# Optimization experiments

Hardware: AMD Instinct MI355X
Metric: run time of the kernel (lower is better)

## Reference

```python
import jax, jax.numpy as jnp
import numpy as np

PNUM = 1024

def _smooth_l1(d):
    ad = jnp.abs(d)
    return jnp.where(ad < 1.0, 0.5 * d * d, ad - 0.5)

def setup_inputs() -> dict:
    key = jax.random.key(0)
    k1, k2 = jax.random.split(key)
    B = 128
    pred = jax.random.normal(k1, (B, PNUM, 2), dtype=jnp.float32)
    gt = jax.random.normal(k2, (B, PNUM, 2), dtype=jnp.float32)
    return {"pred": pred, "gt": gt}

def reference(pred, gt):
    pnum = pred.shape[1]
    # idx[i, j] = (j + i) % pnum : all cyclic shifts of gt point ordering
    idx = (jnp.arange(pnum)[:, None] + jnp.arange(pnum)[None, :]) % pnum
    gt_expand = gt[:, idx, :]                 # [B, pnum, pnum, 2]
    diff = pred[:, None, :, :] - gt_expand    # broadcast over shift axis
    dis = _smooth_l1(diff).sum(axis=3).mean(axis=2)  # [B, pnum]
    min_dis = jnp.min(dis, axis=1)            # [B]; per-sample mean of [1,1] is itself
    return jnp.mean(min_dis)
```

## Files before the change

### kernel.cpp

```cpp
#include <hip/hip_runtime.h>

#define PNUM 1024
#define NB   128
#define PAD(k) ((k) + ((k) >> 2))

typedef _Float16 h2 __attribute__((ext_vector_type(2)));

#define SL1(acc, p, g) do {                               \
    h2 d_ = (p) - (g);                                    \
    h2 a_ = __builtin_elementwise_abs(d_);                \
    h2 m_ = __builtin_elementwise_min(a_, one2);          \
    h2 t_ = __builtin_elementwise_fma(m_, nh2, a_);       \
    (acc) = __builtin_elementwise_fma(m_, t_, (acc)); } while (0)

static __device__ __forceinline__ h2 to_h2(float2 f) {
  h2 r; r.x = (_Float16)f.x; r.y = (_Float16)f.y; return r;
}

__global__ __launch_bounds__(256) void poly_cost_kernel(
    const float* __restrict__ pred, const float* __restrict__ gt,
    float* __restrict__ block_min) {
  __shared__ h2    pred_s[1280];
  __shared__ h2    gt_s[1360];
  __shared__ float partial[16][64];

  const int b     = blockIdx.x >> 4;
  const int chunk = blockIdx.x & 15;
  const int t     = threadIdx.x;

  const float2* pred2 = (const float2*)(pred + (size_t)b * (PNUM * 2));
  const float2* gt2   = (const float2*)(gt   + (size_t)b * (PNUM * 2));

  #pragma unroll
  for (int k = t; k < PNUM; k += 256)
    pred_s[PAD(k)] = to_h2(pred2[k]);
  const int gb = chunk * 64;
  for (int k = t; k < 1088; k += 256)
    gt_s[PAD(k)] = to_h2(gt2[(gb + k) & (PNUM - 1)]);
  __syncthreads();

  const int sslot = t & 15;
  const int jslot = t >> 4;
  const int kbase = sslot * 4 + jslot * 64;
  int A = PAD(kbase);
  int P = PAD(jslot * 64);

  const h2 one2 = { (_Float16)1.0f,  (_Float16)1.0f };
  const h2 nh2  = { (_Float16)-0.5f, (_Float16)-0.5f };
  h2 acc0 = { (_Float16)0.0f, (_Float16)0.0f };
  h2 acc1 = acc0, acc2 = acc0, acc3 = acc0;

  h2 w0 = gt_s[A], w1 = gt_s[A + 1], w2 = gt_s[A + 2];

  for (int g = 0; g < 16; ++g) {
    h2 p0 = pred_s[P];
    h2 w3 = gt_s[A + 3];
    SL1(acc0, p0, w0); SL1(acc1, p0, w1); SL1(acc2, p0, w2); SL1(acc3, p0, w3);
    h2 p1 = pred_s[P + 1];
    h2 n0 = gt_s[A + 5];
    SL1(acc0, p1, w1); SL1(acc1, p1, w2); SL1(acc2, p1, w3); SL1(acc3, p1, n0);
    h2 p2 = pred_s[P + 2];
    h2 n1 = gt_s[A + 6];
    SL1(acc0, p2, w2); SL1(acc1, p2, w3); SL1(acc2, p2, n0); SL1(acc3, p2, n1);
    h2 p3 = pred_s[P + 3];
    h2 n2 = gt_s[A + 7];
    SL1(acc0, p3, w3); SL1(acc1, p3, n0); SL1(acc2, p3, n1); SL1(acc3, p3, n2);
    w0 = n0; w1 = n1; w2 = n2;
    A += 5; P += 5;
  }

  {
    const int ls = sslot * 4;
    partial[jslot][ls + 0] = (float)acc0.x + (float)acc0.y;
    partial[jslot][ls + 1] = (float)acc1.x + (float)acc1.y;
    partial[jslot][ls + 2] = (float)acc2.x + (float)acc2.y;
    partial[jslot][ls + 3] = (float)acc3.x + (float)acc3.y;
  }
  __syncthreads();

  if (t < 64) {
    float s = 0.0f;
    #pragma unroll
    for (int q = 0; q < 16; ++q) s += partial[q][t];
    float dis = s * (1.0f / 1024.0f);
    #pragma unroll
    for (int off = 32; off; off >>= 1)
      dis = fminf(dis, __shfl_xor(dis, off));
    if (t == 0) block_min[blockIdx.x] = dis;
  }
}

__global__ __launch_bounds__(128) void poly_reduce_kernel(
    const float* __restrict__ block_min, float* __restrict__ out) {
  const int b = threadIdx.x;
  float m = block_min[b * 16];
  #pragma unroll
  for (int c = 1; c < 16; ++c) m = fminf(m, block_min[b * 16 + c]);
  #pragma unroll
  for (int off = 32; off; off >>= 1) m += __shfl_xor(m, off);
  __shared__ float wsum[2];
  if ((b & 63) == 0) wsum[b >> 6] = m;
  __syncthreads();
  if (b == 0) out[0] = (wsum[0] + wsum[1]) * (1.0f / NB);
}

extern "C" void kernel_launch(void* const* d_in, const int* in_sizes, int n_in,
                              void* d_out, int out_size, void* d_ws, size_t ws_size,
                              hipStream_t stream) {
  const float* pred = (const float*)d_in[0];
  const float* gt   = (const float*)d_in[1];
  float* out        = (float*)d_out;
  float* block_min  = (float*)d_ws;

  poly_cost_kernel<<<NB * 16, 256, 0, stream>>>(pred, gt, block_min);
  poly_reduce_kernel<<<1, 128, 0, stream>>>(block_min, out);
}
```

Baseline: 29.32 us.

## Fuse final reduction into cost kernel via last-block atomic counter

Replaces the separate reduction kernel launch with a last-block-done pattern: each block publishes its minimum with a release store and increments an atomic counter, and the final block performs the batch mean. The pred shared-memory layout also changes to 66-stride rows so each thread reads its four pred values with two 8-byte vector loads instead of four scalar loads. This removes a kernel launch and trims LDS instructions, but adds a memset before the kernel, an atomic per block and an extra barrier.

```diff
diff --git a/kernel.cpp b/kernel.cpp
--- a/kernel.cpp
+++ b/kernel.cpp
@@ -1,10 +1,13 @@
 #include <hip/hip_runtime.h>
 
-#define PNUM 1024
-#define NB   128
-#define PAD(k) ((k) + ((k) >> 2))
+#define PNUM    1024
+#define NB      128
+#define NBLOCKS (NB * 16)
 
 typedef _Float16 h2 __attribute__((ext_vector_type(2)));
+typedef _Float16 h4 __attribute__((ext_vector_type(4)));
+
+#define PAD(k) ((k) + ((k) >> 2))
 
 #define SL1(acc, p, g) do {                               \
     h2 d_ = (p) - (g);                                    \
@@ -17,12 +20,14 @@
   h2 r; r.x = (_Float16)f.x; r.y = (_Float16)f.y; return r;
 }
 
-__global__ __launch_bounds__(256) void poly_cost_kernel(
+__global__ __launch_bounds__(256) void poly_kernel(
     const float* __restrict__ pred, const float* __restrict__ gt,
-    float* __restrict__ block_min) {
-  __shared__ h2    pred_s[1280];
+    float* __restrict__ block_min, unsigned* __restrict__ counter,
+    float* __restrict__ out) {
+  __shared__ h2    pred_s[1054];
   __shared__ h2    gt_s[1360];
   __shared__ float partial[16][64];
+  __shared__ int   lastflag;
 
   const int b     = blockIdx.x >> 4;
   const int chunk = blockIdx.x & 15;
@@ -33,7 +38,7 @@
 
   #pragma unroll
   for (int k = t; k < PNUM; k += 256)
-    pred_s[PAD(k)] = to_h2(pred2[k]);
+    pred_s[66 * (k >> 6) + (k & 63)] = to_h2(pred2[k]);
   const int gb = chunk * 64;
   for (int k = t; k < 1088; k += 256)
     gt_s[PAD(k)] = to_h2(gt2[(gb + k) & (PNUM - 1)]);
@@ -41,40 +46,38 @@
 
   const int sslot = t & 15;
   const int jslot = t >> 4;
-  const int kbase = sslot * 4 + jslot * 64;
-  int A = PAD(kbase);
-  int P = PAD(jslot * 64);
+  const h2* Pp = pred_s + 66 * jslot;
+  const h2* Gp = gt_s + PAD(4 * sslot + 64 * jslot);
 
-  const h2 one2 = { (_Float16)1.0f,  (_Float16)1.0f };
-  const h2 nh2  = { (_Float16)-0.5f, (_Float16)-0.5f };
-  h2 acc0 = { (_Float16)0.0f, (_Float16)0.0f };
-  h2 acc1 = acc0, acc2 = acc0, acc3 = acc0;
+  const h2 one2 = {(_Float16)1.0f,  (_Float16)1.0f};
+  const h2 nh2  = {(_Float16)-0.5f, (_Float16)-0.5f};
+  h2 a0 = {(_Float16)0.0f, (_Float16)0.0f};
+  h2 a1 = a0, a2 = a0, a3 = a0;
 
-  h2 w0 = gt_s[A], w1 = gt_s[A + 1], w2 = gt_s[A + 2];
+  h2 w0 = Gp[0], w1 = Gp[1], w2 = Gp[2];
 
   for (int g = 0; g < 16; ++g) {
-    h2 p0 = pred_s[P];
-    h2 w3 = gt_s[A + 3];
-    SL1(acc0, p0, w0); SL1(acc1, p0, w1); SL1(acc2, p0, w2); SL1(acc3, p0, w3);
-    h2 p1 = pred_s[P + 1];
-    h2 n0 = gt_s[A + 5];
-    SL1(acc0, p1, w1); SL1(acc1, p1, w2); SL1(acc2, p1, w3); SL1(acc3, p1, n0);
-    h2 p2 = pred_s[P + 2];
-    h2 n1 = gt_s[A + 6];
-    SL1(acc0, p2, w2); SL1(acc1, p2, w3); SL1(acc2, p2, n0); SL1(acc3, p2, n1);
-    h2 p3 = pred_s[P + 3];
-    h2 n2 = gt_s[A + 7];
-    SL1(acc0, p3, w3); SL1(acc1, p3, n0); SL1(acc2, p3, n1); SL1(acc3, p3, n2);
+    h4 pa = *(const h4*)(Pp);
+    h4 pb = *(const h4*)(Pp + 2);
+    h2 p0 = pa.xy, p1 = pa.zw, p2 = pb.xy, p3 = pb.zw;
+    h2 w3 = Gp[3];
+    SL1(a0, p0, w0); SL1(a1, p0, w1); SL1(a2, p0, w2); SL1(a3, p0, w3);
+    h2 n0 = Gp[5];
+    SL1(a0, p1, w1); SL1(a1, p1, w2); SL1(a2, p1, w3); SL1(a3, p1, n0);
+    h2 n1 = Gp[6];
+    SL1(a0, p2, w2); SL1(a1, p2, w3); SL1(a2, p2, n0); SL1(a3, p2, n1);
+    h2 n2 = Gp[7];
+    SL1(a0, p3, w3); SL1(a1, p3, n0); SL1(a2, p3, n1); SL1(a3, p3, n2);
     w0 = n0; w1 = n1; w2 = n2;
-    A += 5; P += 5;
+    Gp += 5; Pp += 4;
   }
 
   {
     const int ls = sslot * 4;
-    partial[jslot][ls + 0] = (float)acc0.x + (float)acc0.y;
-    partial[jslot][ls + 1] = (float)acc1.x + (float)acc1.y;
-    partial[jslot][ls + 2] = (float)acc2.x + (float)acc2.y;
-    partial[jslot][ls + 3] = (float)acc3.x + (float)acc3.y;
+    partial[jslot][ls + 0] = (float)a0.x + (float)a0.y;
+    partial[jslot][ls + 1] = (float)a1.x + (float)a1.y;
+    partial[jslot][ls + 2] = (float)a2.x + (float)a2.y;
+    partial[jslot][ls + 3] = (float)a3.x + (float)a3.y;
   }
   __syncthreads();
 
@@ -86,22 +89,34 @@
     #pragma unroll
     for (int off = 32; off; off >>= 1)
       dis = fminf(dis, __shfl_xor(dis, off));
-    if (t == 0) block_min[blockIdx.x] = dis;
+    if (t == 0) {
+      __hip_atomic_store(&block_min[blockIdx.x], dis,
+                         __ATOMIC_RELEASE, __HIP_MEMORY_SCOPE_AGENT);
+      unsigned old = __hip_atomic_fetch_add(counter, 1u,
+                         __ATOMIC_ACQ_REL, __HIP_MEMORY_SCOPE_AGENT);
+      lastflag = (old == NBLOCKS - 1);
+    }
   }
-}
+  __syncthreads();
 
-__global__ __launch_bounds__(128) void poly_reduce_kernel(
-    const float* __restrict__ block_min, float* __restrict__ out) {
-  const int b = threadIdx.x;
-  float m = block_min[b * 16];
-  #pragma unroll
-  for (int c = 1; c < 16; ++c) m = fminf(m, block_min[b * 16 + c]);
-  #pragma unroll
-  for (int off = 32; off; off >>= 1) m += __shfl_xor(m, off);
-  __shared__ float wsum[2];
-  if ((b & 63) == 0) wsum[b >> 6] = m;
-  __syncthreads();
-  if (b == 0) out[0] = (wsum[0] + wsum[1]) * (1.0f / NB);
+  if (lastflag) {
+    float m = 0.0f;
+    if (t < NB) {
+      m = __hip_atomic_load(&block_min[t * 16],
+                            __ATOMIC_ACQUIRE, __HIP_MEMORY_SCOPE_AGENT);
+      #pragma unroll
+      for (int c = 1; c < 16; ++c) {
+        float v = __hip_atomic_load(&block_min[t * 16 + c],
+                                    __ATOMIC_ACQUIRE, __HIP_MEMORY_SCOPE_AGENT);
+        m = fminf(m, v);
+      }
+    }
+    #pragma unroll
+    for (int off = 32; off; off >>= 1) m += __shfl_xor(m, off);
+    if (t < NB && (t & 63) == 0) partial[0][t >> 6] = m;
+    __syncthreads();
+    if (t == 0) out[0] = (partial[0][0] + partial[0][1]) * (1.0f / NB);
+  }
 }
 
 extern "C" void kernel_launch(void* const* d_in, const int* in_sizes, int n_in,
@@ -111,7 +126,8 @@
   const float* gt   = (const float*)d_in[1];
   float* out        = (float*)d_out;
   float* block_min  = (float*)d_ws;
+  unsigned* counter = (unsigned*)((char*)d_ws + NBLOCKS * 4);
 
-  poly_cost_kernel<<<NB * 16, 256, 0, stream>>>(pred, gt, block_min);
-  poly_reduce_kernel<<<1, 128, 0, stream>>>(block_min, out);
+  hipMemsetAsync(counter, 0, 4, stream);
+  poly_kernel<<<NBLOCKS, 256, 0, stream>>>(pred, gt, block_min, counter, out);
 }
```

Measured after the change: 68.58 us. 134% more time.
